# Optimization experiments

Hardware: AMD Instinct MI355X
Metric: run time of the kernel (lower is better)

The kernel has to match this reference:

```python
import jax, jax.numpy as jnp
import numpy as np

B, CIN, COUT, K, H, W = 8, 256, 256, 4, 128, 128
BN_EPS = 1e-5


def setup_inputs() -> dict:
    key = jax.random.key(0)
    ks = jax.random.split(key, 12)
    n = lambda i, shape, scale: jax.random.normal(ks[i], shape, jnp.float32) * scale
    return {
        "x": jax.random.normal(ks[0], (B, CIN, H, W), jnp.float32),
        "conv_w": n(1, (COUT, CIN), 0.05),
        "conv_b": n(2, (COUT,), 0.02),
        "off_w": n(3, (K, 2, CIN), 0.02),   # k offset convs, each 1x1 -> 2 channels
        "off_b": n(4, (K, 2), 0.02),
        "wgt_w": n(5, (K, CIN), 0.05),      # weight conv 1x1 -> k channels (softmax over k)
        "wgt_b": n(6, (K,), 0.02),
        "gamma": 1.0 + n(7, (COUT,), 0.1),
        "beta": n(8, (COUT,), 0.1),
        "run_mean": n(9, (COUT,), 0.05),
        "run_var": 1.0 + 0.1 * jax.random.uniform(ks[10], (COUT,), jnp.float32),
        "out_w": n(11, (CIN, COUT), 0.05),
        "out_b": jnp.zeros((CIN,), jnp.float32),
    }


def bilinear_sample(img, gx, gy):
    """F.grid_sample(mode='bilinear', padding_mode='zeros', align_corners=True).
    img: [B,C,H,W]; gx,gy: [B,H,W] normalized coords in [-1,1]."""
    b, c, h, w = img.shape
    x = (gx + 1.0) * 0.5 * (w - 1)  # unnormalize (align_corners=True)
    y = (gy + 1.0) * 0.5 * (h - 1)
    x0 = jnp.floor(x)
    y0 = jnp.floor(y)
    wx1 = x - x0
    wy1 = y - y0
    imgf = img.reshape(b, c, h * w)

    def gather(xi, yi, wgt):
        valid = (xi >= 0) & (xi <= w - 1) & (yi >= 0) & (yi <= h - 1)
        xic = jnp.clip(xi, 0, w - 1).astype(jnp.int32)
        yic = jnp.clip(yi, 0, h - 1).astype(jnp.int32)
        idx = (yic * w + xic).reshape(b, 1, h * w)
        v = jnp.take_along_axis(imgf, idx, axis=2).reshape(b, c, h, w)
        return v * (wgt * valid)[:, None]  # zeros padding: OOB corners contribute 0

    return (gather(x0, y0, (1 - wx1) * (1 - wy1))
            + gather(x0 + 1, y0, wx1 * (1 - wy1))
            + gather(x0, y0 + 1, (1 - wx1) * wy1)
            + gather(x0 + 1, y0 + 1, wx1 * wy1))


def reference(x, conv_w, conv_b, off_w, off_b, wgt_w, wgt_b,
              gamma, beta, run_mean, run_var, out_w, out_b):
    # 1x1 projection conv
    proj = jnp.einsum('bchw,oc->bohw', x, conv_w) + conv_b[:, None, None]
    # k offset branches at once: [K,B,2,H,W]
    flows = jnp.einsum('bchw,koc->kbohw', x, off_w) + off_b[:, None, :, None, None]
    # per-branch softmax weights: [B,K,H,W]
    logits = jnp.einsum('bchw,kc->bkhw', x, wgt_w) + wgt_b[None, :, None, None]
    weights = jax.nn.softmax(logits, axis=1)
    # base grid + flow, normalized to [-1,1]
    grid_x = jnp.arange(W, dtype=jnp.float32)[None, None, None, :]  # broadcast over k,b,h
    grid_y = jnp.arange(H, dtype=jnp.float32)[None, None, :, None]
    vx = grid_x + flows[:, :, 0]  # [K,B,H,W]
    vy = grid_y + flows[:, :, 1]
    gxn = 2.0 * vx / max(W - 1, 1) - 1.0
    gyn = 2.0 * vy / max(H - 1, 1) - 1.0
    feats = jax.vmap(lambda gx, gy: bilinear_sample(proj, gx, gy))(gxn, gyn)  # [K,B,C,H,W]
    # repeat_interleave(weights, out_ch) * cat(feats) then split+sum == weighted sum over k
    fsum = jnp.einsum('kbchw,bkhw->bchw', feats, weights)
    feat = proj + fsum  # dropout in eval mode = identity
    # BatchNorm2d (eval: running stats)
    inv = gamma / jnp.sqrt(run_var + BN_EPS)
    feat = (feat - run_mean[:, None, None]) * inv[:, None, None] + beta[:, None, None]
    return jnp.einsum('bchw,oc->bohw', feat, out_w) + out_b[:, None, None]
```

## Files before the change

### kernel.cpp

```cpp
#include <hip/hip_runtime.h>
#include <cstddef>
#include <cstdint>

#define B_    8
#define CIN_  256
#define COUT_ 256
#define K_    4
#define H_    128
#define W_    128
#define HW_   (H_ * W_)
#define P_    (B_ * HW_)
#define BN_EPS 1e-5f

typedef __attribute__((ext_vector_type(8))) short bf16x8_t;
typedef __attribute__((ext_vector_type(4))) float f32x4_t;

__device__ __forceinline__ unsigned short f2bf(float f) {
    unsigned int u = __float_as_uint(f);
    u += 0x7fffu + ((u >> 16) & 1u);
    return (unsigned short)(u >> 16);
}
__device__ __forceinline__ float bf2f_lo(unsigned int u) { return __uint_as_float(u << 16); }
__device__ __forceinline__ float bf2f_hi(unsigned int u) { return __uint_as_float(u & 0xffff0000u); }

#define GL2LDS(g, l)                                                                     \
    __builtin_amdgcn_global_load_lds((const __attribute__((address_space(1))) void*)(g), \
                                     (__attribute__((address_space(3))) void*)(l), 16, 0, 0)

__global__ __launch_bounds__(256) void k_wcast(
    const float* __restrict__ w0, const float* __restrict__ w1,
    unsigned short* __restrict__ o0, unsigned short* __restrict__ o1)
{
    const int i = (blockIdx.x * 256 + threadIdx.x) * 4;
    float4 a = *(const float4*)&w0[i];
    float4 b = *(const float4*)&w1[i];
    uint2 pa, pb;
    pa.x = (unsigned)f2bf(a.x) | ((unsigned)f2bf(a.y) << 16);
    pa.y = (unsigned)f2bf(a.z) | ((unsigned)f2bf(a.w) << 16);
    pb.x = (unsigned)f2bf(b.x) | ((unsigned)f2bf(b.y) << 16);
    pb.y = (unsigned)f2bf(b.z) | ((unsigned)f2bf(b.w) << 16);
    *(uint2*)&o0[i] = pa;
    *(uint2*)&o1[i] = pb;
}

__global__ __launch_bounds__(256) void k_flows(
    const float* __restrict__ x, const float* __restrict__ off_w,
    const float* __restrict__ off_b, const float* __restrict__ wgt_w,
    const float* __restrict__ wgt_b, unsigned short* __restrict__ xT,
    float* __restrict__ coords, float* __restrict__ swts)
{
    __shared__ float coef[12 * 256];
    __shared__ alignas(16) unsigned short tile[256 * 68];
    const int t = threadIdx.x;
    for (int idx = t; idx < 12 * 256; idx += 256)
        coef[idx] = (idx < 8 * 256) ? off_w[idx] : wgt_w[idx - 8 * 256];
    __syncthreads();

    const int p  = blockIdx.x * 256 + t;
    const int b  = p >> 14;
    const int hw = p & (HW_ - 1);
    const float* xp = x + (size_t)b * (256 * HW_) + hw;
    const int px0 = blockIdx.x * 256;

    float acc[12];
#pragma unroll
    for (int j = 0; j < 12; ++j) acc[j] = 0.f;

    for (int chunk = 0; chunk < 4; ++chunk) {
        const int cbase = chunk * 64;
#pragma unroll 4
        for (int cc = 0; cc < 64; ++cc) {
            const float xv = xp[(size_t)(cbase + cc) * HW_];
            tile[t * 68 + cc] = f2bf(xv);
#pragma unroll
            for (int j = 0; j < 12; ++j)
                acc[j] = fmaf(xv, coef[j * 256 + cbase + cc], acc[j]);
        }
        __syncthreads();
#pragma unroll
        for (int pass = 0; pass < 16; ++pass) {
            const int px = pass * 16 + (t >> 4);
            const int j4 = (t & 15) * 4;
            const uint2 v = *(const uint2*)&tile[px * 68 + j4];
            *(uint2*)&xT[(size_t)(px0 + px) * 256 + cbase + j4] = v;
        }
        __syncthreads();
    }

    const int w = hw & (W_ - 1);
    const int h = hw >> 7;
    float l[4];
#pragma unroll
    for (int k = 0; k < 4; ++k) {
        const float fx = acc[k * 2 + 0] + off_b[k * 2 + 0];
        const float fy = acc[k * 2 + 1] + off_b[k * 2 + 1];
        coords[(size_t)p * 8 + k * 2 + 0] = (float)w + fx;
        coords[(size_t)p * 8 + k * 2 + 1] = (float)h + fy;
        l[k] = acc[8 + k] + wgt_b[k];
    }
    const float m  = fmaxf(fmaxf(l[0], l[1]), fmaxf(l[2], l[3]));
    const float e0 = __expf(l[0] - m), e1 = __expf(l[1] - m);
    const float e2 = __expf(l[2] - m), e3 = __expf(l[3] - m);
    const float inv = 1.f / (e0 + e1 + e2 + e3);
    swts[(size_t)p * 4 + 0] = e0 * inv;
    swts[(size_t)p * 4 + 1] = e1 * inv;
    swts[(size_t)p * 4 + 2] = e2 * inv;
    swts[(size_t)p * 4 + 3] = e3 * inv;
}

#define GEMM_STAGE_AND_MFMA(A_, W_ptr_, smem_)                                              \
    char* As = smem_;                                                                       \
    char* Bs = smem_ + 16384;                                                               \
    const int w  = t >> 6;                                                                  \
    const int l  = t & 63;                                                                  \
    const int lr = l & 15;                                                                  \
    const int lq = l >> 4;                                                                  \
    f32x4_t acc[4][4];                                                                      \
    _Pragma("unroll") for (int i = 0; i < 4; ++i)                                           \
        _Pragma("unroll") for (int j = 0; j < 4; ++j)                                       \
            acc[i][j] = (f32x4_t){0.f, 0.f, 0.f, 0.f};                                      \
    const int wm = (w & 1) * 4;                                                             \
    const int wn = (w >> 1) * 4;                                                            \
    _Pragma("unroll") for (int ks = 0; ks < 4; ++ks) {                                      \
        const int k0 = ks * 64;                                                             \
        __syncthreads();                                                                    \
        _Pragma("unroll") for (int i = 0; i < 2; ++i) {                                     \
            const int mt = 2 * w + i;                                                       \
            _Pragma("unroll") for (int kc = 0; kc < 2; ++kc) {                              \
                const unsigned short* g =                                                   \
                    A_ + (size_t)(p0 + mt * 16 + lr) * 256 + k0 + kc * 32 + lq * 8;         \
                GL2LDS(g, As + (kc * 8 + mt) * 1024);                                       \
            }                                                                               \
        }                                                                                   \
        _Pragma("unroll") for (int i = 0; i < 2; ++i) {                                     \
            const int nt = 2 * w + i;                                                       \
            _Pragma("unroll") for (int kc = 0; kc < 2; ++kc) {                              \
                const unsigned short* g =                                                   \
                    W_ptr_ + (size_t)(n0 + nt * 16 + lr) * 256 + k0 + kc * 32 + lq * 8;     \
                GL2LDS(g, Bs + (kc * 8 + nt) * 1024);                                       \
            }                                                                               \
        }                                                                                   \
        __syncthreads();                                                                    \
        _Pragma("unroll") for (int kc = 0; kc < 2; ++kc) {                                  \
            bf16x8_t af[4], bfr[4];                                                         \
            _Pragma("unroll") for (int i = 0; i < 4; ++i)                                   \
                af[i] = *(const bf16x8_t*)(As + (kc * 8 + wm + i) * 1024 + l * 16);         \
            _Pragma("unroll") for (int j = 0; j < 4; ++j)                                   \
                bfr[j] = *(const bf16x8_t*)(Bs + (kc * 8 + wn + j) * 1024 + l * 16);        \
            _Pragma("unroll") for (int i = 0; i < 4; ++i)                                   \
                _Pragma("unroll") for (int j = 0; j < 4; ++j)                               \
                    acc[i][j] =                                                             \
                        __builtin_amdgcn_mfma_f32_16x16x32_bf16(af[i], bfr[j], acc[i][j],   \
                                                                0, 0, 0);                   \
        }                                                                                   \
    }

__global__ __launch_bounds__(256, 2) void k_proj(
    const unsigned short* __restrict__ A, const unsigned short* __restrict__ Wb,
    const float* __restrict__ bias, unsigned short* __restrict__ Cout)
{
    __shared__ alignas(16) char smem[33792];
    const int t  = threadIdx.x;
    const int bx = blockIdx.x;
    const int n0 = (bx & 1) * 128;
    const int p0 = (bx >> 1) * 128;

    GEMM_STAGE_AND_MFMA(A, Wb, smem)

    __syncthreads();
    unsigned short* ep = (unsigned short*)smem;
    const int mh = (w & 1) * 64, nh = (w >> 1) * 64;
#pragma unroll
    for (int j = 0; j < 4; ++j) {
        const int   col = nh + j * 16 + lr;
        const float bv  = bias[n0 + col];
#pragma unroll
        for (int i = 0; i < 4; ++i) {
#pragma unroll
            for (int r = 0; r < 4; ++r) {
                const int row = mh + i * 16 + lq * 4 + r;
                ep[row * 132 + col] = f2bf(acc[i][j][r] + bv);
            }
        }
    }
    __syncthreads();
#pragma unroll
    for (int pass = 0; pass < 16; ++pass) {
        const int row = pass * 8 + (t >> 5);
        const int c4  = (t & 31) * 4;
        const uint2 v = *(const uint2*)&ep[row * 132 + c4];
        *(uint2*)&Cout[(size_t)(p0 + row) * 256 + n0 + c4] = v;
    }
}

__global__ __launch_bounds__(256, 2) void k_out(
    const unsigned short* __restrict__ A, const unsigned short* __restrict__ Wb,
    const float* __restrict__ bias, float* __restrict__ Cout)
{
    __shared__ alignas(16) char smem[32768];
    const int t  = threadIdx.x;
    const int bx = blockIdx.x;
    const int n0 = (bx & 1) * 128;
    const int p0 = (bx >> 1) * 128;

    GEMM_STAGE_AND_MFMA(A, Wb, smem)

    const int mh = (w & 1) * 64, nh = (w >> 1) * 64;
    const int b   = p0 >> 14;
    const int hw0 = p0 & (HW_ - 1);
#pragma unroll
    for (int j = 0; j < 4; ++j) {
        const int   n  = n0 + nh + j * 16 + lr;
        const float bb = bias[n];
#pragma unroll
        for (int i = 0; i < 4; ++i) {
            f32x4_t v = acc[i][j];
            v[0] += bb; v[1] += bb; v[2] += bb; v[3] += bb;
            *(f32x4_t*)&Cout[(size_t)(b * 256 + n) * HW_ + hw0 + mh + i * 16 + lq * 4] = v;
        }
    }
}

__global__ __launch_bounds__(256) void k_sample(
    const unsigned short* __restrict__ proj, const float* __restrict__ coords,
    const float* __restrict__ swts,
    const float* __restrict__ gamma, const float* __restrict__ beta,
    const float* __restrict__ rmean, const float* __restrict__ rvar,
    unsigned short* __restrict__ feat)
{
    const int t  = threadIdx.x;
    const int t7 = t & 127;
    const int ph = t >> 7;
    const int c  = t7 * 2;
    const float2 mn = *(const float2*)&rmean[c];
    const float2 vr = *(const float2*)&rvar[c];
    const float2 gm = *(const float2*)&gamma[c];
    const float2 bt = *(const float2*)&beta[c];
    const float inv0 = gm.x * rsqrtf(vr.x + BN_EPS);
    const float inv1 = gm.y * rsqrtf(vr.y + BN_EPS);

    const int pbase = blockIdx.x * 8;
    const int b = pbase >> 14;
    const unsigned short* projb = proj + (size_t)b * HW_ * 256;

#pragma unroll
    for (int it = 0; it < 4; ++it) {
        const int p = pbase + it * 2 + ph;
        const unsigned int sv = *(const unsigned int*)&proj[(size_t)p * 256 + c];
        float a0 = bf2f_lo(sv & 0xffffu);
        float a1 = bf2f_hi(sv);
#pragma unroll
        for (int k = 0; k < 4; ++k) {
            const float sx = coords[(size_t)p * 8 + k * 2 + 0];
            const float sy = coords[(size_t)p * 8 + k * 2 + 1];
            const float wk = swts[(size_t)p * 4 + k];
            const float x0f = floorf(sx), y0f = floorf(sy);
            const float fx = sx - x0f, fy = sy - y0f;
            const float vx0 = (x0f >= 0.f && x0f <= (float)(W_ - 1)) ? 1.f : 0.f;
            const float vx1 = (x0f >= -1.f && x0f <= (float)(W_ - 2)) ? 1.f : 0.f;
            const float vy0 = (y0f >= 0.f && y0f <= (float)(H_ - 1)) ? 1.f : 0.f;
            const float vy1 = (y0f >= -1.f && y0f <= (float)(H_ - 2)) ? 1.f : 0.f;
            const int x0 = (int)x0f, y0 = (int)y0f;
            const int cx0 = min(max(x0, 0), W_ - 1);
            const int cx1 = min(max(x0 + 1, 0), W_ - 1);
            const int cy0 = min(max(y0, 0), H_ - 1);
            const int cy1 = min(max(y0 + 1, 0), H_ - 1);
            const float w00 = (1.f - fx) * (1.f - fy) * wk * vx0 * vy0;
            const float w10 = fx * (1.f - fy) * wk * vx1 * vy0;
            const float w01 = (1.f - fx) * fy * wk * vx0 * vy1;
            const float w11 = fx * fy * wk * vx1 * vy1;
            const unsigned int v00 = *(const unsigned int*)&projb[(size_t)(cy0 * W_ + cx0) * 256 + c];
            const unsigned int v10 = *(const unsigned int*)&projb[(size_t)(cy0 * W_ + cx1) * 256 + c];
            const unsigned int v01 = *(const unsigned int*)&projb[(size_t)(cy1 * W_ + cx0) * 256 + c];
            const unsigned int v11 = *(const unsigned int*)&projb[(size_t)(cy1 * W_ + cx1) * 256 + c];
            a0 = fmaf(w00, bf2f_lo(v00 & 0xffffu), a0);
            a1 = fmaf(w00, bf2f_hi(v00), a1);
            a0 = fmaf(w10, bf2f_lo(v10 & 0xffffu), a0);
            a1 = fmaf(w10, bf2f_hi(v10), a1);
            a0 = fmaf(w01, bf2f_lo(v01 & 0xffffu), a0);
            a1 = fmaf(w01, bf2f_hi(v01), a1);
            a0 = fmaf(w11, bf2f_lo(v11 & 0xffffu), a0);
            a1 = fmaf(w11, bf2f_hi(v11), a1);
        }
        const float r0 = (a0 - mn.x) * inv0 + bt.x;
        const float r1 = (a1 - mn.y) * inv1 + bt.y;
        const unsigned int o = (unsigned)f2bf(r0) | ((unsigned)f2bf(r1) << 16);
        *(unsigned int*)&feat[(size_t)p * 256 + c] = o;
    }
}

extern "C" void kernel_launch(void* const* d_in, const int* in_sizes, int n_in,
                              void* d_out, int out_size, void* d_ws, size_t ws_size,
                              hipStream_t stream)
{
    const float* x      = (const float*)d_in[0];
    const float* conv_w = (const float*)d_in[1];
    const float* conv_b = (const float*)d_in[2];
    const float* off_w  = (const float*)d_in[3];
    const float* off_b  = (const float*)d_in[4];
    const float* wgt_w  = (const float*)d_in[5];
    const float* wgt_b  = (const float*)d_in[6];
    const float* gamma  = (const float*)d_in[7];
    const float* beta   = (const float*)d_in[8];
    const float* rmean  = (const float*)d_in[9];
    const float* rvar   = (const float*)d_in[10];
    const float* out_w  = (const float*)d_in[11];
    const float* out_b  = (const float*)d_in[12];

    char* ws = (char*)d_ws;
    unsigned short* xT     = (unsigned short*)(ws);
    unsigned short* proj   = (unsigned short*)(ws + (size_t)67108864);
    unsigned short* feat   = (unsigned short*)(ws + (size_t)134217728);
    float*          coords = (float*)(ws + (size_t)201326592);
    float*          swts   = (float*)(ws + (size_t)205520896);
    unsigned short* wA     = (unsigned short*)(ws + (size_t)207618048);
    unsigned short* wB     = (unsigned short*)(ws + (size_t)207749120);

    k_wcast <<<64,          256, 0, stream>>>(conv_w, out_w, wA, wB);
    k_flows <<<P_ / 256,    256, 0, stream>>>(x, off_w, off_b, wgt_w, wgt_b, xT, coords, swts);
    k_proj  <<<(P_/128)*2,  256, 0, stream>>>(xT, wA, conv_b, proj);
    k_sample<<<P_ / 8,      256, 0, stream>>>(proj, coords, swts, gamma, beta, rmean, rvar, feat);
    k_out   <<<(P_/128)*2,  256, 0, stream>>>(feat, wB, out_b, (float*)d_out);
}
```

Before: 456.6 us.

## Fold BatchNorm into output GEMM weights and precompute bilinear sample tables

The eval-mode BatchNorm scale is folded into the bf16 output weights and its shift into a new output bias, so the sampling kernel no longer applies the affine per element. The flows kernel now computes the bilinear corner weights (including the softmax weight and zero-padding masks) and the clamped gather offsets once per pixel and branch, and stores them as float4/int4 tables. k_sample is rewritten so each thread handles 8 channels with 16-byte gathers instead of 2 channels with 4-byte gathers. The GEMM launch bounds are raised to 3 blocks per CU. This trades larger table traffic for fewer redundant index computations and wider loads, and it risks register spills in the GEMMs and slightly different rounding because BN is now applied inside bf16 weights.

```diff
diff --git a/kernel.cpp b/kernel.cpp
--- a/kernel.cpp
+++ b/kernel.cpp
@@ -20,34 +20,58 @@
     u += 0x7fffu + ((u >> 16) & 1u);
     return (unsigned short)(u >> 16);
 }
-__device__ __forceinline__ float bf2f_lo(unsigned int u) { return __uint_as_float(u << 16); }
-__device__ __forceinline__ float bf2f_hi(unsigned int u) { return __uint_as_float(u & 0xffff0000u); }
+__device__ __forceinline__ float2 up2(unsigned int u) {
+    return make_float2(__uint_as_float(u << 16), __uint_as_float(u & 0xffff0000u));
+}
+__device__ __forceinline__ void fma2(float2& d, float s, float2 v) {
+    d.x = fmaf(s, v.x, d.x);
+    d.y = fmaf(s, v.y, d.y);
+}
 
 #define GL2LDS(g, l)                                                                     \
     __builtin_amdgcn_global_load_lds((const __attribute__((address_space(1))) void*)(g), \
                                      (__attribute__((address_space(3))) void*)(l), 16, 0, 0)
 
-__global__ __launch_bounds__(256) void k_wcast(
-    const float* __restrict__ w0, const float* __restrict__ w1,
-    unsigned short* __restrict__ o0, unsigned short* __restrict__ o1)
-{
-    const int i = (blockIdx.x * 256 + threadIdx.x) * 4;
-    float4 a = *(const float4*)&w0[i];
-    float4 b = *(const float4*)&w1[i];
-    uint2 pa, pb;
-    pa.x = (unsigned)f2bf(a.x) | ((unsigned)f2bf(a.y) << 16);
-    pa.y = (unsigned)f2bf(a.z) | ((unsigned)f2bf(a.w) << 16);
-    pb.x = (unsigned)f2bf(b.x) | ((unsigned)f2bf(b.y) << 16);
-    pb.y = (unsigned)f2bf(b.z) | ((unsigned)f2bf(b.w) << 16);
-    *(uint2*)&o0[i] = pa;
-    *(uint2*)&o1[i] = pb;
+__global__ __launch_bounds__(256) void k_prep(
+    const float* __restrict__ conv_w, const float* __restrict__ out_w,
+    const float* __restrict__ gamma, const float* __restrict__ beta,
+    const float* __restrict__ rmean, const float* __restrict__ rvar,
+    const float* __restrict__ out_b,
+    unsigned short* __restrict__ wA, unsigned short* __restrict__ wB,
+    float* __restrict__ bias2)
+{
+    const int t = threadIdx.x;
+    if (blockIdx.x < 64) {
+        const int i = (blockIdx.x * 256 + t) * 4;
+        float4 a = *(const float4*)&conv_w[i];
+        uint2 pa;
+        pa.x = (unsigned)f2bf(a.x) | ((unsigned)f2bf(a.y) << 16);
+        pa.y = (unsigned)f2bf(a.z) | ((unsigned)f2bf(a.w) << 16);
+        *(uint2*)&wA[i] = pa;
+    } else {
+        __shared__ float sinv[256], sd[256];
+        const float iv = gamma[t] * rsqrtf(rvar[t] + BN_EPS);
+        sinv[t] = iv;
+        sd[t]   = beta[t] - rmean[t] * iv;
+        __syncthreads();
+        float acc = out_b[t];
+        for (int c = 0; c < 256; c += 4) {
+            const float4 wv = *(const float4*)&out_w[t * 256 + c];
+            acc += sd[c] * wv.x + sd[c + 1] * wv.y + sd[c + 2] * wv.z + sd[c + 3] * wv.w;
+            uint2 p;
+            p.x = (unsigned)f2bf(wv.x * sinv[c])     | ((unsigned)f2bf(wv.y * sinv[c + 1]) << 16);
+            p.y = (unsigned)f2bf(wv.z * sinv[c + 2]) | ((unsigned)f2bf(wv.w * sinv[c + 3]) << 16);
+            *(uint2*)&wB[t * 256 + c] = p;
+        }
+        bias2[t] = acc;
+    }
 }
 
 __global__ __launch_bounds__(256) void k_flows(
     const float* __restrict__ x, const float* __restrict__ off_w,
     const float* __restrict__ off_b, const float* __restrict__ wgt_w,
     const float* __restrict__ wgt_b, unsigned short* __restrict__ xT,
-    float* __restrict__ coords, float* __restrict__ swts)
+    float4* __restrict__ tabW, int4* __restrict__ tabI)
 {
     __shared__ float coef[12 * 256];
     __shared__ alignas(16) unsigned short tile[256 * 68];
@@ -91,21 +115,41 @@
     const int h = hw >> 7;
     float l[4];
 #pragma unroll
-    for (int k = 0; k < 4; ++k) {
-        const float fx = acc[k * 2 + 0] + off_b[k * 2 + 0];
-        const float fy = acc[k * 2 + 1] + off_b[k * 2 + 1];
-        coords[(size_t)p * 8 + k * 2 + 0] = (float)w + fx;
-        coords[(size_t)p * 8 + k * 2 + 1] = (float)h + fy;
-        l[k] = acc[8 + k] + wgt_b[k];
-    }
+    for (int k = 0; k < 4; ++k) l[k] = acc[8 + k] + wgt_b[k];
     const float m  = fmaxf(fmaxf(l[0], l[1]), fmaxf(l[2], l[3]));
     const float e0 = __expf(l[0] - m), e1 = __expf(l[1] - m);
     const float e2 = __expf(l[2] - m), e3 = __expf(l[3] - m);
-    const float inv = 1.f / (e0 + e1 + e2 + e3);
-    swts[(size_t)p * 4 + 0] = e0 * inv;
-    swts[(size_t)p * 4 + 1] = e1 * inv;
-    swts[(size_t)p * 4 + 2] = e2 * inv;
-    swts[(size_t)p * 4 + 3] = e3 * inv;
+    const float sinv = 1.f / (e0 + e1 + e2 + e3);
+    float wk[4] = {e0 * sinv, e1 * sinv, e2 * sinv, e3 * sinv};
+
+#pragma unroll
+    for (int k = 0; k < 4; ++k) {
+        const float sx = (float)w + acc[k * 2 + 0] + off_b[k * 2 + 0];
+        const float sy = (float)h + acc[k * 2 + 1] + off_b[k * 2 + 1];
+        const float x0f = floorf(sx), y0f = floorf(sy);
+        const float fx = sx - x0f, fy = sy - y0f;
+        const float vx0 = (x0f >= 0.f  && x0f <= (float)(W_ - 1)) ? 1.f : 0.f;
+        const float vx1 = (x0f >= -1.f && x0f <= (float)(W_ - 2)) ? 1.f : 0.f;
+        const float vy0 = (y0f >= 0.f  && y0f <= (float)(H_ - 1)) ? 1.f : 0.f;
+        const float vy1 = (y0f >= -1.f && y0f <= (float)(H_ - 2)) ? 1.f : 0.f;
+        const int x0 = (int)x0f, y0 = (int)y0f;
+        const int cx0 = min(max(x0, 0), W_ - 1);
+        const int cx1 = min(max(x0 + 1, 0), W_ - 1);
+        const int cy0 = min(max(y0, 0), H_ - 1);
+        const int cy1 = min(max(y0 + 1, 0), H_ - 1);
+        float4 wv;
+        wv.x = (1.f - fx) * (1.f - fy) * wk[k] * vx0 * vy0;
+        wv.y = fx * (1.f - fy) * wk[k] * vx1 * vy0;
+        wv.z = (1.f - fx) * fy * wk[k] * vx0 * vy1;
+        wv.w = fx * fy * wk[k] * vx1 * vy1;
+        int4 ov;
+        ov.x = (cy0 * W_ + cx0) * 256;
+        ov.y = (cy0 * W_ + cx1) * 256;
+        ov.z = (cy1 * W_ + cx0) * 256;
+        ov.w = (cy1 * W_ + cx1) * 256;
+        tabW[(size_t)k * P_ + p] = wv;
+        tabI[(size_t)k * P_ + p] = ov;
+    }
 }
 
 #define GEMM_STAGE_AND_MFMA(A_, W_ptr_, smem_)                                              \
@@ -155,7 +199,7 @@
         }                                                                                   \
     }
 
-__global__ __launch_bounds__(256, 2) void k_proj(
+__global__ __launch_bounds__(256, 3) void k_proj(
     const unsigned short* __restrict__ A, const unsigned short* __restrict__ Wb,
     const float* __restrict__ bias, unsigned short* __restrict__ Cout)
 {
@@ -193,7 +237,7 @@
     }
 }
 
-__global__ __launch_bounds__(256, 2) void k_out(
+__global__ __launch_bounds__(256, 3) void k_out(
     const unsigned short* __restrict__ A, const unsigned short* __restrict__ Wb,
     const float* __restrict__ bias, float* __restrict__ Cout)
 {
@@ -222,70 +266,47 @@
 }
 
 __global__ __launch_bounds__(256) void k_sample(
-    const unsigned short* __restrict__ proj, const float* __restrict__ coords,
-    const float* __restrict__ swts,
-    const float* __restrict__ gamma, const float* __restrict__ beta,
-    const float* __restrict__ rmean, const float* __restrict__ rvar,
-    unsigned short* __restrict__ feat)
+    const unsigned short* __restrict__ proj, const float4* __restrict__ tabW,
+    const int4* __restrict__ tabI, unsigned short* __restrict__ feat)
 {
     const int t  = threadIdx.x;
-    const int t7 = t & 127;
-    const int ph = t >> 7;
-    const int c  = t7 * 2;
-    const float2 mn = *(const float2*)&rmean[c];
-    const float2 vr = *(const float2*)&rvar[c];
-    const float2 gm = *(const float2*)&gamma[c];
-    const float2 bt = *(const float2*)&beta[c];
-    const float inv0 = gm.x * rsqrtf(vr.x + BN_EPS);
-    const float inv1 = gm.y * rsqrtf(vr.y + BN_EPS);
-
-    const int pbase = blockIdx.x * 8;
+    const int w  = t >> 6;
+    const int l  = t & 63;
+    const int ph = l >> 5;
+    const int c0 = (l & 31) * 8;
+
+    const int pbase = blockIdx.x * 16;
     const int b = pbase >> 14;
     const unsigned short* projb = proj + (size_t)b * HW_ * 256;
 
 #pragma unroll
-    for (int it = 0; it < 4; ++it) {
-        const int p = pbase + it * 2 + ph;
-        const unsigned int sv = *(const unsigned int*)&proj[(size_t)p * 256 + c];
-        float a0 = bf2f_lo(sv & 0xffffu);
-        float a1 = bf2f_hi(sv);
+    for (int it = 0; it < 2; ++it) {
+        const int p = pbase + it * 8 + w * 2 + ph;
+        const uint4 rv = *(const uint4*)&proj[(size_t)p * 256 + c0];
+        float2 a0 = up2(rv.x), a1 = up2(rv.y), a2 = up2(rv.z), a3 = up2(rv.w);
 #pragma unroll
         for (int k = 0; k < 4; ++k) {
-            const float sx = coords[(size_t)p * 8 + k * 2 + 0];
-            const float sy = coords[(size_t)p * 8 + k * 2 + 1];
-            const float wk = swts[(size_t)p * 4 + k];
-            const float x0f = floorf(sx), y0f = floorf(sy);
-            const float fx = sx - x0f, fy = sy - y0f;
-            const float vx0 = (x0f >= 0.f && x0f <= (float)(W_ - 1)) ? 1.f : 0.f;
-            const float vx1 = (x0f >= -1.f && x0f <= (float)(W_ - 2)) ? 1.f : 0.f;
-            const float vy0 = (y0f >= 0.f && y0f <= (float)(H_ - 1)) ? 1.f : 0.f;
-            const float vy1 = (y0f >= -1.f && y0f <= (float)(H_ - 2)) ? 1.f : 0.f;
-            const int x0 = (int)x0f, y0 = (int)y0f;
-            const int cx0 = min(max(x0, 0), W_ - 1);
-            const int cx1 = min(max(x0 + 1, 0), W_ - 1);
-            const int cy0 = min(max(y0, 0), H_ - 1);
-            const int cy1 = min(max(y0 + 1, 0), H_ - 1);
-            const float w00 = (1.f - fx) * (1.f - fy) * wk * vx0 * vy0;
-            const float w10 = fx * (1.f - fy) * wk * vx1 * vy0;
-            const float w01 = (1.f - fx) * fy * wk * vx0 * vy1;
-            const float w11 = fx * fy * wk * vx1 * vy1;
-            const unsigned int v00 = *(const unsigned int*)&projb[(size_t)(cy0 * W_ + cx0) * 256 + c];
-            const unsigned int v10 = *(const unsigned int*)&projb[(size_t)(cy0 * W_ + cx1) * 256 + c];
-            const unsigned int v01 = *(const unsigned int*)&projb[(size_t)(cy1 * W_ + cx0) * 256 + c];
-            const unsigned int v11 = *(const unsigned int*)&projb[(size_t)(cy1 * W_ + cx1) * 256 + c];
-            a0 = fmaf(w00, bf2f_lo(v00 & 0xffffu), a0);
-            a1 = fmaf(w00, bf2f_hi(v00), a1);
-            a0 = fmaf(w10, bf2f_lo(v10 & 0xffffu), a0);
-            a1 = fmaf(w10, bf2f_hi(v10), a1);
-            a0 = fmaf(w01, bf2f_lo(v01 & 0xffffu), a0);
-            a1 = fmaf(w01, bf2f_hi(v01), a1);
-            a0 = fmaf(w11, bf2f_lo(v11 & 0xffffu), a0);
-            a1 = fmaf(w11, bf2f_hi(v11), a1);
-        }
-        const float r0 = (a0 - mn.x) * inv0 + bt.x;
-        const float r1 = (a1 - mn.y) * inv1 + bt.y;
-        const unsigned int o = (unsigned)f2bf(r0) | ((unsigned)f2bf(r1) << 16);
-        *(unsigned int*)&feat[(size_t)p * 256 + c] = o;
+            const float4 wv = tabW[(size_t)k * P_ + p];
+            const int4   ov = tabI[(size_t)k * P_ + p];
+            const uint4 g0 = *(const uint4*)&projb[ov.x + c0];
+            const uint4 g1 = *(const uint4*)&projb[ov.y + c0];
+            const uint4 g2 = *(const uint4*)&projb[ov.z + c0];
+            const uint4 g3 = *(const uint4*)&projb[ov.w + c0];
+            fma2(a0, wv.x, up2(g0.x)); fma2(a1, wv.x, up2(g0.y));
+            fma2(a2, wv.x, up2(g0.z)); fma2(a3, wv.x, up2(g0.w));
+            fma2(a0, wv.y, up2(g1.x)); fma2(a1, wv.y, up2(g1.y));
+            fma2(a2, wv.y, up2(g1.z)); fma2(a3, wv.y, up2(g1.w));
+            fma2(a0, wv.z, up2(g2.x)); fma2(a1, wv.z, up2(g2.y));
+            fma2(a2, wv.z, up2(g2.z)); fma2(a3, wv.z, up2(g2.w));
+            fma2(a0, wv.w, up2(g3.x)); fma2(a1, wv.w, up2(g3.y));
+            fma2(a2, wv.w, up2(g3.z)); fma2(a3, wv.w, up2(g3.w));
+        }
+        uint4 o;
+        o.x = (unsigned)f2bf(a0.x) | ((unsigned)f2bf(a0.y) << 16);
+        o.y = (unsigned)f2bf(a1.x) | ((unsigned)f2bf(a1.y) << 16);
+        o.z = (unsigned)f2bf(a2.x) | ((unsigned)f2bf(a2.y) << 16);
+        o.w = (unsigned)f2bf(a3.x) | ((unsigned)f2bf(a3.y) << 16);
+        *(uint4*)&feat[(size_t)p * 256 + c0] = o;
     }
 }
 
@@ -308,17 +329,19 @@
     const float* out_b  = (const float*)d_in[12];
 
     char* ws = (char*)d_ws;
-    unsigned short* xT     = (unsigned short*)(ws);
-    unsigned short* proj   = (unsigned short*)(ws + (size_t)67108864);
-    unsigned short* feat   = (unsigned short*)(ws + (size_t)134217728);
-    float*          coords = (float*)(ws + (size_t)201326592);
-    float*          swts   = (float*)(ws + (size_t)205520896);
-    unsigned short* wA     = (unsigned short*)(ws + (size_t)207618048);
-    unsigned short* wB     = (unsigned short*)(ws + (size_t)207749120);
-
-    k_wcast <<<64,          256, 0, stream>>>(conv_w, out_w, wA, wB);
-    k_flows <<<P_ / 256,    256, 0, stream>>>(x, off_w, off_b, wgt_w, wgt_b, xT, coords, swts);
-    k_proj  <<<(P_/128)*2,  256, 0, stream>>>(xT, wA, conv_b, proj);
-    k_sample<<<P_ / 8,      256, 0, stream>>>(proj, coords, swts, gamma, beta, rmean, rvar, feat);
-    k_out   <<<(P_/128)*2,  256, 0, stream>>>(feat, wB, out_b, (float*)d_out);
-}
+    unsigned short* xT   = (unsigned short*)(ws);
+    unsigned short* proj = (unsigned short*)(ws + (size_t)67108864);
+    unsigned short* feat = (unsigned short*)(ws + (size_t)134217728);
+    float4*         tabW = (float4*)(ws + (size_t)201326592);
+    int4*           tabI = (int4*)(ws + (size_t)209715200);
+    unsigned short* wA   = (unsigned short*)(ws + (size_t)218103808);
+    unsigned short* wB   = (unsigned short*)(ws + (size_t)218234880);
+    float*          bias2= (float*)(ws + (size_t)218365952);
+
+    k_prep  <<<65,         256, 0, stream>>>(conv_w, out_w, gamma, beta, rmean, rvar,
+                                             out_b, wA, wB, bias2);
+    k_flows <<<P_ / 256,   256, 0, stream>>>(x, off_w, off_b, wgt_w, wgt_b, xT, tabW, tabI);
+    k_proj  <<<(P_/128)*2, 256, 0, stream>>>(xT, wA, conv_b, proj);
+    k_sample<<<P_ / 16,    256, 0, stream>>>(proj, tabW, tabI, feat);
+    k_out   <<<(P_/128)*2, 256, 0, stream>>>(feat, wB, bias2, (float*)d_out);
+}
```

After: 426.3 us. 6.6% less time.
